# Kernel tuning notes

Hardware: AMD Instinct MI355X
Metric: run time of the kernel (lower is better)

Reference implementation:

```python
import jax, jax.numpy as jnp
import numpy as np

N_NODES = 100000
N_EDGES = 1250000
HID = 64
IN_CH = 64
OUT_CH = 16
N_GRAPHS = 512


def setup_inputs() -> dict:
    key = jax.random.key(0)
    ks = jax.random.split(key, 20)
    x = jax.random.normal(ks[0], (N_NODES, IN_CH), dtype=jnp.float32)
    edge_index = jax.random.randint(ks[1], (2, N_EDGES), 0, N_NODES, dtype=jnp.int64)
    batch = jnp.sort(jax.random.randint(ks[2], (N_NODES,), 0, N_GRAPHS, dtype=jnp.int64))
    s_in = 1.0 / np.sqrt(IN_CH)
    s_h = 1.0 / np.sqrt(HID)
    u = lambda k, shp, s: jax.random.uniform(k, shp, jnp.float32, -s, s)
    return {
        "x": x, "edge_index": edge_index, "batch": batch,
        "W0": u(ks[3], (IN_CH, HID), s_in), "b0": u(ks[4], (HID,), s_in),
        "W1a": u(ks[5], (HID, HID), s_h), "b1a": u(ks[6], (HID,), s_h),
        "W1b": u(ks[7], (HID, HID), s_h), "b1b": u(ks[8], (HID,), s_h),
        "W2a": u(ks[9], (HID, HID), s_h), "b2a": u(ks[10], (HID,), s_h),
        "W2b": u(ks[11], (HID, HID), s_h), "b2b": u(ks[12], (HID,), s_h),
        "W3a": u(ks[13], (HID, HID), s_h), "b3a": u(ks[14], (HID,), s_h),
        "W3b": u(ks[15], (HID, HID), s_h), "b3b": u(ks[16], (HID,), s_h),
        "Wl": u(ks[17], (HID, OUT_CH), s_h), "bl": u(ks[18], (OUT_CH,), s_h),
    }


def _gin_conv(h, src, dst, Wa, ba, Wb, bb):
    # GINConv, eps=0: mlp(x_i + sum_{j->i} x_j); mlp = Linear,ReLU,Linear
    agg = jax.ops.segment_sum(h[src], dst, num_segments=N_NODES)  # [N, HID]
    z = h + agg
    return jax.nn.relu(z @ Wa + ba) @ Wb + bb


def reference(x, edge_index, batch, W0, b0, W1a, b1a, W1b, b1b,
              W2a, b2a, W2b, b2b, W3a, b3a, W3b, b3b, Wl, bl):
    src, dst = edge_index[0], edge_index[1]
    h = jax.nn.relu(x @ W0 + b0)
    h = jax.nn.relu(_gin_conv(h, src, dst, W1a, b1a, W1b, b1b))
    h = jax.nn.relu(_gin_conv(h, src, dst, W2a, b2a, W2b, b2b))
    h = jax.nn.relu(_gin_conv(h, src, dst, W3a, b3a, W3b, b3b))
    # global mean pool over graphs
    sums = jax.ops.segment_sum(h, batch, num_segments=N_GRAPHS)  # [G, HID]
    cnts = jax.ops.segment_sum(jnp.ones((N_NODES,), h.dtype), batch, num_segments=N_GRAPHS)
    pooled = sums / jnp.maximum(cnts, 1.0)[:, None]
    # dropout p=0.5 is identity in eval mode
    return pooled @ Wl + bl  # [G, OUT_CH]
```

## Files before the change

### kernel.cpp

```cpp
#include <hip/hip_runtime.h>
#include <hip/hip_fp16.h>

#define N_NODES 100000
#define N_EDGES 1250000
#define HID 64
#define N_GRAPHS 512
#define OUT_CH 16

#define NSUP 196
#define SB_CAP 8192
#define E_BLK 2048
#define NPB ((N_EDGES + E_BLK - 1) / E_BLK)
#define TILE2 ((N_NODES + 127) / 128)
#define NWP 6
#define TSTRIDE 68
#define AGG_BLOCKS 3125

typedef _Float16 h16;
typedef _Float16 half2_t __attribute__((ext_vector_type(2)));
typedef _Float16 f16x8 __attribute__((ext_vector_type(8)));
typedef float f32x4 __attribute__((ext_vector_type(4)));

__device__ __forceinline__ void acc8(uint4 u, float* a) {
    half2_t h0 = __builtin_bit_cast(half2_t, u.x);
    half2_t h1 = __builtin_bit_cast(half2_t, u.y);
    half2_t h2 = __builtin_bit_cast(half2_t, u.z);
    half2_t h3 = __builtin_bit_cast(half2_t, u.w);
    a[0] += (float)h0[0]; a[1] += (float)h0[1];
    a[2] += (float)h1[0]; a[3] += (float)h1[1];
    a[4] += (float)h2[0]; a[5] += (float)h2[1];
    a[6] += (float)h3[0]; a[7] += (float)h3[1];
}

__device__ __forceinline__ unsigned pack2(float x, float y) {
    half2_t o;
    o[0] = (h16)x;
    o[1] = (h16)y;
    return __builtin_bit_cast(unsigned, o);
}

__global__ __launch_bounds__(256) void k_fat(const int* __restrict__ src,
                                             const int* __restrict__ dst,
                                             int* __restrict__ cnt,
                                             int* __restrict__ buckets,
                                             const float* __restrict__ W1a,
                                             const float* __restrict__ W1b,
                                             const float* __restrict__ W2a,
                                             const float* __restrict__ W2b,
                                             const float* __restrict__ W3a,
                                             const float* __restrict__ W3b,
                                             h16* __restrict__ WF,
                                             const float* __restrict__ W0,
                                             const float* __restrict__ B0,
                                             const float* __restrict__ Xin,
                                             h16* __restrict__ Hout) {
    __shared__ int hist[256];
    __shared__ int gbase[256];
    __shared__ int tsum[256];
    __shared__ __align__(16) int stage[E_BLK];
    __shared__ __align__(16) float sT[4 * 16 * TSTRIDE];

    int b = blockIdx.x;
    int t = threadIdx.x;

    if (b < NPB) {
        int e0 = b * E_BLK;
        int eN = N_EDGES - e0;
        if (eN > E_BLK) eN = E_BLK;

        hist[t] = 0;
        __syncthreads();
        for (int i = t; i < eN; i += 256) atomicAdd(&hist[dst[e0 + i] >> 9], 1);
        __syncthreads();

        int c = hist[t];
        tsum[t] = c;
        __syncthreads();
        for (int off = 1; off < 256; off <<= 1) {
            int u = (t >= off) ? tsum[t - off] : 0;
            __syncthreads();
            tsum[t] += u;
            __syncthreads();
        }
        int pref = tsum[t] - c;
        if (t < NSUP && c > 0) gbase[t] = atomicAdd(&cnt[t], c);
        hist[t] = pref;
        __syncthreads();

        for (int i = t; i < eN; i += 256) {
            int s = src[e0 + i];
            int d = dst[e0 + i];
            int p = atomicAdd(&hist[d >> 9], 1);
            stage[p] = ((d & 511) << 17) | s;
        }
        __syncthreads();

        if (t < NSUP && c > 0) {
            int lstart = hist[t] - c;
            int gb = gbase[t];
            int cap = SB_CAP - gb;
            int n = c < cap ? c : (cap > 0 ? cap : 0);
            int* dp = buckets + (size_t)t * SB_CAP + gb;
            int r = 0;
            while (r < n && (((size_t)(dp + r)) & 15)) { dp[r] = stage[lstart + r]; ++r; }
            for (; r + 4 <= n; r += 4) {
                int4 v;
                v.x = stage[lstart + r];
                v.y = stage[lstart + r + 1];
                v.z = stage[lstart + r + 2];
                v.w = stage[lstart + r + 3];
                *(int4*)(dp + r) = v;
            }
            for (; r < n; ++r) dp[r] = stage[lstart + r];
        }
    } else if (b < NPB + NWP) {
        const float* Ws[NWP] = {W1a, W1b, W2a, W2b, W3a, W3b};
        const float* W = Ws[b - NPB];
        h16* dstW = WF + (size_t)(b - NPB) * 4096;
#pragma unroll
        for (int i = 0; i < 16; ++i) {
            int s = t + 256 * i;
            int k = s >> 6, col = s & 63;
            int kc = k >> 5, quad = (k >> 3) & 3, j = k & 7;
            int c = col >> 4, n = col & 15;
            dstW[((c * 2 + kc) * 4 + quad) * 128 + n * 8 + j] = (h16)W[s];
        }
    } else {
        int lb = b - NPB - NWP;
        int w = t >> 6, lane = t & 63;
        int n16 = lane & 15, quad = lane >> 4;
        float* T = sT + w * 16 * TSTRIDE;

        f16x8 bw[4][2];
#pragma unroll
        for (int c = 0; c < 4; ++c)
#pragma unroll
            for (int kc = 0; kc < 2; ++kc) {
                f16x8 v;
#pragma unroll
                for (int j = 0; j < 8; ++j)
                    v[j] = (h16)W0[(kc * 32 + quad * 8 + j) * 64 + c * 16 + n16];
                bw[c][kc] = v;
            }
        float bv[4];
#pragma unroll
        for (int c = 0; c < 4; ++c) bv[c] = B0[c * 16 + n16];

#pragma unroll
        for (int tt = 0; tt < 2; ++tt) {
            int rbase = lb * 128 + tt * 64 + w * 16;
            int arow = rbase + n16;
            int crow = arow < N_NODES ? arow : N_NODES - 1;
            f16x8 a[2];
#pragma unroll
            for (int kc = 0; kc < 2; ++kc) {
                const float4* xp = (const float4*)(Xin + (size_t)crow * HID + kc * 32 + quad * 8);
                float4 p = xp[0], q = xp[1];
                f16x8 v;
                v[0] = (h16)p.x; v[1] = (h16)p.y; v[2] = (h16)p.z; v[3] = (h16)p.w;
                v[4] = (h16)q.x; v[5] = (h16)q.y; v[6] = (h16)q.z; v[7] = (h16)q.w;
                a[kc] = v;
            }

            f32x4 acc[4];
#pragma unroll
            for (int c = 0; c < 4; ++c) {
                acc[c] = (f32x4){bv[c], bv[c], bv[c], bv[c]};
#pragma unroll
                for (int kc = 0; kc < 2; ++kc)
                    acc[c] = __builtin_amdgcn_mfma_f32_16x16x32_f16(a[kc], bw[c][kc], acc[c], 0, 0, 0);
            }

#pragma unroll
            for (int c = 0; c < 4; ++c)
#pragma unroll
                for (int r = 0; r < 4; ++r)
                    T[(quad * 4 + r) * TSTRIDE + c * 16 + n16] = fmaxf(acc[c][r], 0.f);
            {
                int rl = lane >> 2, seg = lane & 3;
                int row = rbase + rl;
                if (row < N_NODES) {
                    const float* tr = &T[rl * TSTRIDE + seg * 16];
                    f16x8 o0, o1;
#pragma unroll
                    for (int i = 0; i < 8; ++i) {
                        o0[i] = (h16)tr[i];
                        o1[i] = (h16)tr[8 + i];
                    }
                    f16x8* dp = (f16x8*)(Hout + (size_t)row * HID + seg * 16);
                    dp[0] = o0;
                    dp[1] = o1;
                }
            }
        }
    }
}

__global__ __launch_bounds__(256) void k_sort(const int* __restrict__ cnt,
                                              int* __restrict__ buckets,
                                              int* __restrict__ rowptrS) {
    __shared__ int srt[SB_CAP];
    __shared__ int hist[512];
    __shared__ int curs[512];
    __shared__ int tsum[256];
    int s = blockIdx.x, t = threadIdx.x;
    int n = cnt[s];
    n = n < SB_CAP ? n : SB_CAP;
    int* gb = buckets + (size_t)s * SB_CAP;
    int sBase = s * SB_CAP;

    hist[t] = 0;
    hist[t + 256] = 0;
    __syncthreads();
    for (int i = t; i < n; i += 256) atomicAdd(&hist[gb[i] >> 17], 1);
    __syncthreads();

    int c0 = hist[2 * t], c1 = hist[2 * t + 1];
    int tot = c0 + c1;
    tsum[t] = tot;
    __syncthreads();
    for (int off = 1; off < 256; off <<= 1) {
        int u = (t >= off) ? tsum[t - off] : 0;
        __syncthreads();
        tsum[t] += u;
        __syncthreads();
    }
    int pref = tsum[t] - tot;
    curs[2 * t] = pref;
    curs[2 * t + 1] = pref + c0;
    rowptrS[s * 513 + 2 * t] = sBase + pref;
    rowptrS[s * 513 + 2 * t + 1] = sBase + pref + c0;
    if (t == 255) rowptrS[s * 513 + 512] = sBase + n;
    __syncthreads();

    for (int i = t; i < n; i += 256) {
        int rec = gb[i];
        int pos = atomicAdd(&curs[rec >> 17], 1);
        srt[pos] = rec;
    }
    __syncthreads();
    for (int i = t; i < n; i += 256) gb[i] = srt[i];
}

__global__ __launch_bounds__(256) void k_aggregate(const int* __restrict__ rowptrS,
                                                   const int* __restrict__ buckets,
                                                   const h16* __restrict__ H,
                                                   h16* __restrict__ Z) {
    const uint4* H8 = (const uint4*)H;
    uint4* Z8 = (uint4*)Z;
    int lane = threadIdx.x & 63;
    int part = lane >> 3, sub = lane & 7;
    int gwave = (blockIdx.x * 256 + threadIdx.x) >> 6;
    int nw = (gridDim.x * 256) >> 6;
    for (int i0 = gwave * 8; i0 < N_NODES; i0 += nw * 8) {
        int i = i0 + part;
        bool valid = i < N_NODES;
        int iv = valid ? i : N_NODES - 1;
        int s = iv >> 9, l = iv & 511;
        int start = rowptrS[s * 513 + l];
        int end = valid ? rowptrS[s * 513 + l + 1] : start;
        float a[8] = {0.f, 0.f, 0.f, 0.f, 0.f, 0.f, 0.f, 0.f};
        acc8(H8[(size_t)iv * 8 + sub], a);
        int j = start;
        for (; j + 8 <= end; j += 8) {
            int s0 = buckets[j] & 0x1FFFF;
            int s1 = buckets[j + 1] & 0x1FFFF;
            int s2 = buckets[j + 2] & 0x1FFFF;
            int s3 = buckets[j + 3] & 0x1FFFF;
            int s4 = buckets[j + 4] & 0x1FFFF;
            int s5 = buckets[j + 5] & 0x1FFFF;
            int s6 = buckets[j + 6] & 0x1FFFF;
            int s7 = buckets[j + 7] & 0x1FFFF;
            uint4 u0 = H8[(size_t)s0 * 8 + sub];
            uint4 u1 = H8[(size_t)s1 * 8 + sub];
            uint4 u2 = H8[(size_t)s2 * 8 + sub];
            uint4 u3 = H8[(size_t)s3 * 8 + sub];
            uint4 u4 = H8[(size_t)s4 * 8 + sub];
            uint4 u5 = H8[(size_t)s5 * 8 + sub];
            uint4 u6 = H8[(size_t)s6 * 8 + sub];
            uint4 u7 = H8[(size_t)s7 * 8 + sub];
            acc8(u0, a);
            acc8(u1, a);
            acc8(u2, a);
            acc8(u3, a);
            acc8(u4, a);
            acc8(u5, a);
            acc8(u6, a);
            acc8(u7, a);
        }
        if (j + 4 <= end) {
            int s0 = buckets[j] & 0x1FFFF;
            int s1 = buckets[j + 1] & 0x1FFFF;
            int s2 = buckets[j + 2] & 0x1FFFF;
            int s3 = buckets[j + 3] & 0x1FFFF;
            uint4 u0 = H8[(size_t)s0 * 8 + sub];
            uint4 u1 = H8[(size_t)s1 * 8 + sub];
            uint4 u2 = H8[(size_t)s2 * 8 + sub];
            uint4 u3 = H8[(size_t)s3 * 8 + sub];
            acc8(u0, a);
            acc8(u1, a);
            acc8(u2, a);
            acc8(u3, a);
            j += 4;
        }
        if (j + 2 <= end) {
            int s0 = buckets[j] & 0x1FFFF;
            int s1 = buckets[j + 1] & 0x1FFFF;
            uint4 u0 = H8[(size_t)s0 * 8 + sub];
            uint4 u1 = H8[(size_t)s1 * 8 + sub];
            acc8(u0, a);
            acc8(u1, a);
            j += 2;
        }
        if (j < end) {
            int s0 = buckets[j] & 0x1FFFF;
            acc8(H8[(size_t)s0 * 8 + sub], a);
        }
        if (valid) {
            uint4 o;
            o.x = pack2(a[0], a[1]);
            o.y = pack2(a[2], a[3]);
            o.z = pack2(a[4], a[5]);
            o.w = pack2(a[6], a[7]);
            Z8[(size_t)i * 8 + sub] = o;
        }
    }
}

__global__ __launch_bounds__(256) void k_mlp(const h16* __restrict__ WaF,
                                             const float* __restrict__ Ba,
                                             const h16* __restrict__ WbF,
                                             const float* __restrict__ Bb,
                                             const h16* __restrict__ Zin,
                                             h16* __restrict__ Hout) {
    __shared__ __align__(16) float sT[4 * 16 * TSTRIDE];
    int t = threadIdx.x;
    int w = t >> 6, lane = t & 63;
    int n16 = lane & 15, quad = lane >> 4;
    float* T = sT + w * 16 * TSTRIDE;

    f16x8 bwa[4][2], bwb[4][2];
#pragma unroll
    for (int c = 0; c < 4; ++c)
#pragma unroll
        for (int kc = 0; kc < 2; ++kc) {
            int f = ((c * 2 + kc) * 4 + quad) * 128 + n16 * 8;
            bwa[c][kc] = *(const f16x8*)(WaF + f);
            bwb[c][kc] = *(const f16x8*)(WbF + f);
        }
    float bva[4], bvb[4];
#pragma unroll
    for (int c = 0; c < 4; ++c) {
        bva[c] = Ba[c * 16 + n16];
        bvb[c] = Bb[c * 16 + n16];
    }

#pragma unroll
    for (int tt = 0; tt < 2; ++tt) {
        int rbase = blockIdx.x * 128 + tt * 64 + w * 16;
        int arow = rbase + n16;
        int crow = arow < N_NODES ? arow : N_NODES - 1;
        const f16x8* zp = (const f16x8*)(Zin + (size_t)crow * HID + quad * 8);
        f16x8 a0 = zp[0];
        f16x8 a1 = zp[4];

        f32x4 acc[4];
#pragma unroll
        for (int c = 0; c < 4; ++c) {
            acc[c] = (f32x4){bva[c], bva[c], bva[c], bva[c]};
            acc[c] = __builtin_amdgcn_mfma_f32_16x16x32_f16(a0, bwa[c][0], acc[c], 0, 0, 0);
            acc[c] = __builtin_amdgcn_mfma_f32_16x16x32_f16(a1, bwa[c][1], acc[c], 0, 0, 0);
        }

#pragma unroll
        for (int c = 0; c < 4; ++c)
#pragma unroll
            for (int r = 0; r < 4; ++r)
                T[(quad * 4 + r) * TSTRIDE + c * 16 + n16] = fmaxf(acc[c][r], 0.f);

        f16x8 ta[2];
#pragma unroll
        for (int kc = 0; kc < 2; ++kc) {
            float4 p = *(const float4*)&T[n16 * TSTRIDE + kc * 32 + quad * 8];
            float4 q = *(const float4*)&T[n16 * TSTRIDE + kc * 32 + quad * 8 + 4];
            f16x8 v;
            v[0] = (h16)p.x; v[1] = (h16)p.y; v[2] = (h16)p.z; v[3] = (h16)p.w;
            v[4] = (h16)q.x; v[5] = (h16)q.y; v[6] = (h16)q.z; v[7] = (h16)q.w;
            ta[kc] = v;
        }

#pragma unroll
        for (int c = 0; c < 4; ++c) {
            acc[c] = (f32x4){bvb[c], bvb[c], bvb[c], bvb[c]};
            acc[c] = __builtin_amdgcn_mfma_f32_16x16x32_f16(ta[0], bwb[c][0], acc[c], 0, 0, 0);
            acc[c] = __builtin_amdgcn_mfma_f32_16x16x32_f16(ta[1], bwb[c][1], acc[c], 0, 0, 0);
        }

#pragma unroll
        for (int c = 0; c < 4; ++c)
#pragma unroll
            for (int r = 0; r < 4; ++r)
                T[(quad * 4 + r) * TSTRIDE + c * 16 + n16] = fmaxf(acc[c][r], 0.f);
        {
            int rl = lane >> 2, seg = lane & 3;
            int row = rbase + rl;
            if (row < N_NODES) {
                const float* tr = &T[rl * TSTRIDE + seg * 16];
                f16x8 o0, o1;
#pragma unroll
                for (int i = 0; i < 8; ++i) {
                    o0[i] = (h16)tr[i];
                    o1[i] = (h16)tr[8 + i];
                }
                f16x8* dp = (f16x8*)(Hout + (size_t)row * HID + seg * 16);
                dp[0] = o0;
                dp[1] = o1;
            }
        }
    }
}

__global__ __launch_bounds__(256) void k_poolfinal(const h16* __restrict__ H,
                                                   const int* __restrict__ batch,
                                                   const float* __restrict__ Wl,
                                                   const float* __restrict__ bl,
                                                   float* __restrict__ out) {
    __shared__ float sp[4 * HID];
    int g = blockIdx.x;
    int t = threadIdx.x;
    int lane = t & 63, w = t >> 6;
    int lo = 0, hi = N_NODES;
    while (lo < hi) { int m = (lo + hi) >> 1; if (batch[m] < g) lo = m + 1; else hi = m; }
    int start = lo;
    hi = N_NODES;
    while (lo < hi) { int m = (lo + hi) >> 1; if (batch[m] < g + 1) lo = m + 1; else hi = m; }
    int end = lo;
    float s0 = 0.f, s1 = 0.f, s2 = 0.f, s3 = 0.f;
    int r = start + w;
    for (; r + 12 < end; r += 16) {
        float v0 = (float)H[(size_t)r * HID + lane];
        float v1 = (float)H[(size_t)(r + 4) * HID + lane];
        float v2 = (float)H[(size_t)(r + 8) * HID + lane];
        float v3 = (float)H[(size_t)(r + 12) * HID + lane];
        s0 += v0; s1 += v1; s2 += v2; s3 += v3;
    }
    for (; r < end; r += 4) s0 += (float)H[(size_t)r * HID + lane];
    sp[w * HID + lane] = s0 + s1 + s2 + s3;
    __syncthreads();
    if (t < HID) {
        float tot = sp[t] + sp[HID + t] + sp[2 * HID + t] + sp[3 * HID + t];
        float c = (end > start) ? (float)(end - start) : 1.0f;
        sp[t] = tot / c;
    }
    __syncthreads();
    if (t < OUT_CH) {
        float acc = bl[t];
#pragma unroll
        for (int k = 0; k < HID; ++k) acc += sp[k] * Wl[k * OUT_CH + t];
        out[g * OUT_CH + t] = acc;
    }
}

extern "C" void kernel_launch(void* const* d_in, const int* in_sizes, int n_in,
                              void* d_out, int out_size, void* d_ws, size_t ws_size,
                              hipStream_t stream) {
    const float* x     = (const float*)d_in[0];
    const int*   edge  = (const int*)d_in[1];
    const int*   batch = (const int*)d_in[2];
    const float* W0  = (const float*)d_in[3];
    const float* b0  = (const float*)d_in[4];
    const float* W1a = (const float*)d_in[5];
    const float* b1a = (const float*)d_in[6];
    const float* W1b = (const float*)d_in[7];
    const float* b1b = (const float*)d_in[8];
    const float* W2a = (const float*)d_in[9];
    const float* b2a = (const float*)d_in[10];
    const float* W2b = (const float*)d_in[11];
    const float* b2b = (const float*)d_in[12];
    const float* W3a = (const float*)d_in[13];
    const float* b3a = (const float*)d_in[14];
    const float* W3b = (const float*)d_in[15];
    const float* b3b = (const float*)d_in[16];
    const float* Wl  = (const float*)d_in[17];
    const float* bl  = (const float*)d_in[18];
    float* out = (float*)d_out;

    const int* src = edge;
    const int* dst = edge + N_EDGES;

    h16* HA = (h16*)d_ws;
    h16* Z  = HA + (size_t)N_NODES * HID;
    int* cnt     = (int*)(Z + (size_t)N_NODES * HID);
    int* rowptrS = cnt + NSUP;
    int* buckets = rowptrS + NSUP * 513;
    h16* WF      = (h16*)(buckets + (size_t)NSUP * SB_CAP);
    h16* W1aF = WF;
    h16* W1bF = WF + 4096 * 1;
    h16* W2aF = WF + 4096 * 2;
    h16* W2bF = WF + 4096 * 3;
    h16* W3aF = WF + 4096 * 4;
    h16* W3bF = WF + 4096 * 5;

    hipMemsetAsync(cnt, 0, NSUP * sizeof(int), stream);
    k_fat<<<NPB + NWP + TILE2, 256, 0, stream>>>(src, dst, cnt, buckets,
        W1a, W1b, W2a, W2b, W3a, W3b, WF, W0, b0, x, HA);
    k_sort<<<NSUP, 256, 0, stream>>>(cnt, buckets, rowptrS);

    k_aggregate<<<AGG_BLOCKS, 256, 0, stream>>>(rowptrS, buckets, HA, Z);
    k_mlp<<<TILE2, 256, 0, stream>>>(W1aF, b1a, W1bF, b1b, Z, HA);

    k_aggregate<<<AGG_BLOCKS, 256, 0, stream>>>(rowptrS, buckets, HA, Z);
    k_mlp<<<TILE2, 256, 0, stream>>>(W2aF, b2a, W2bF, b2b, Z, HA);

    k_aggregate<<<AGG_BLOCKS, 256, 0, stream>>>(rowptrS, buckets, HA, Z);
    k_mlp<<<TILE2, 256, 0, stream>>>(W3aF, b3a, W3bF, b3b, Z, HA);

    k_poolfinal<<<N_GRAPHS, 256, 0, stream>>>(HA, batch, Wl, bl, out);
}
```

Measured before the change: 274.6 us.

## Split first-layer features into column quarters for cache-local gather aggregation

The first hidden activation is now written as four 16-feature column slabs instead of row-major rows. A new quarter-wise aggregation kernel gathers each slab separately, so each pass's random gather touches a much smaller working set and can stay cache-resident. The first MLP reads this split layout through a new flag. Later layers keep the row-major path. The cost is more waves each doing smaller 32-byte gathers, plus repeated index reads across the four quarters.

Result: slower. 298.3 us (+8.6%).

```diff
diff --git a/kernel.cpp b/kernel.cpp
--- a/kernel.cpp
+++ b/kernel.cpp
@@ -15,6 +15,7 @@
 #define NWP 6
 #define TSTRIDE 68
 #define AGG_BLOCKS 3125
+#define QCHUNKS 3125
 
 typedef _Float16 h16;
 typedef _Float16 half2_t __attribute__((ext_vector_type(2)));
@@ -187,9 +188,9 @@
                         o0[i] = (h16)tr[i];
                         o1[i] = (h16)tr[8 + i];
                     }
-                    f16x8* dp = (f16x8*)(Hout + (size_t)row * HID + seg * 16);
-                    dp[0] = o0;
-                    dp[1] = o1;
+                    h16* dp = Hout + (size_t)seg * N_NODES * 16 + (size_t)row * 16;
+                    *(f16x8*)dp = o0;
+                    *(f16x8*)(dp + 8) = o1;
                 }
             }
         }
@@ -240,6 +241,77 @@
     }
     __syncthreads();
     for (int i = t; i < n; i += 256) gb[i] = srt[i];
+}
+
+__global__ __launch_bounds__(256) void k_aggregate_q(const int* __restrict__ rowptrS,
+                                                     const int* __restrict__ buckets,
+                                                     const h16* __restrict__ Hq,
+                                                     h16* __restrict__ Zq) {
+    const uint4* H2 = (const uint4*)Hq;
+    uint4* Z2 = (uint4*)Zq;
+    int lane = threadIdx.x & 63;
+    int sub = lane & 1;
+    int grp = lane >> 1;
+    int gwave = (blockIdx.x * 256 + threadIdx.x) >> 6;
+    int q = gwave / QCHUNKS;
+    int i = (gwave - q * QCHUNKS) * 32 + grp;
+    size_t pb = (size_t)q * N_NODES * 2;
+    int s = i >> 9, l = i & 511;
+    int start = rowptrS[s * 513 + l];
+    int end = rowptrS[s * 513 + l + 1];
+    float a[8] = {0.f, 0.f, 0.f, 0.f, 0.f, 0.f, 0.f, 0.f};
+    acc8(H2[pb + (size_t)i * 2 + sub], a);
+    int j = start;
+    for (; j + 8 <= end; j += 8) {
+        int s0 = buckets[j] & 0x1FFFF;
+        int s1 = buckets[j + 1] & 0x1FFFF;
+        int s2 = buckets[j + 2] & 0x1FFFF;
+        int s3 = buckets[j + 3] & 0x1FFFF;
+        int s4 = buckets[j + 4] & 0x1FFFF;
+        int s5 = buckets[j + 5] & 0x1FFFF;
+        int s6 = buckets[j + 6] & 0x1FFFF;
+        int s7 = buckets[j + 7] & 0x1FFFF;
+        uint4 u0 = H2[pb + (size_t)s0 * 2 + sub];
+        uint4 u1 = H2[pb + (size_t)s1 * 2 + sub];
+        uint4 u2 = H2[pb + (size_t)s2 * 2 + sub];
+        uint4 u3 = H2[pb + (size_t)s3 * 2 + sub];
+        uint4 u4 = H2[pb + (size_t)s4 * 2 + sub];
+        uint4 u5 = H2[pb + (size_t)s5 * 2 + sub];
+        uint4 u6 = H2[pb + (size_t)s6 * 2 + sub];
+        uint4 u7 = H2[pb + (size_t)s7 * 2 + sub];
+        acc8(u0, a); acc8(u1, a); acc8(u2, a); acc8(u3, a);
+        acc8(u4, a); acc8(u5, a); acc8(u6, a); acc8(u7, a);
+    }
+    if (j + 4 <= end) {
+        int s0 = buckets[j] & 0x1FFFF;
+        int s1 = buckets[j + 1] & 0x1FFFF;
+        int s2 = buckets[j + 2] & 0x1FFFF;
+        int s3 = buckets[j + 3] & 0x1FFFF;
+        uint4 u0 = H2[pb + (size_t)s0 * 2 + sub];
+        uint4 u1 = H2[pb + (size_t)s1 * 2 + sub];
+        uint4 u2 = H2[pb + (size_t)s2 * 2 + sub];
+        uint4 u3 = H2[pb + (size_t)s3 * 2 + sub];
+        acc8(u0, a); acc8(u1, a); acc8(u2, a); acc8(u3, a);
+        j += 4;
+    }
+    if (j + 2 <= end) {
+        int s0 = buckets[j] & 0x1FFFF;
+        int s1 = buckets[j + 1] & 0x1FFFF;
+        uint4 u0 = H2[pb + (size_t)s0 * 2 + sub];
+        uint4 u1 = H2[pb + (size_t)s1 * 2 + sub];
+        acc8(u0, a); acc8(u1, a);
+        j += 2;
+    }
+    if (j < end) {
+        int s0 = buckets[j] & 0x1FFFF;
+        acc8(H2[pb + (size_t)s0 * 2 + sub], a);
+    }
+    uint4 o;
+    o.x = pack2(a[0], a[1]);
+    o.y = pack2(a[2], a[3]);
+    o.z = pack2(a[4], a[5]);
+    o.w = pack2(a[6], a[7]);
+    Z2[pb + (size_t)i * 2 + sub] = o;
 }
 
 __global__ __launch_bounds__(256) void k_aggregate(const int* __restrict__ rowptrS,
@@ -332,7 +404,8 @@
                                              const h16* __restrict__ WbF,
                                              const float* __restrict__ Bb,
                                              const h16* __restrict__ Zin,
-                                             h16* __restrict__ Hout) {
+                                             h16* __restrict__ Hout,
+                                             const int qin) {
     __shared__ __align__(16) float sT[4 * 16 * TSTRIDE];
     int t = threadIdx.x;
     int w = t >> 6, lane = t & 63;
@@ -360,9 +433,16 @@
         int rbase = blockIdx.x * 128 + tt * 64 + w * 16;
         int arow = rbase + n16;
         int crow = arow < N_NODES ? arow : N_NODES - 1;
-        const f16x8* zp = (const f16x8*)(Zin + (size_t)crow * HID + quad * 8);
-        f16x8 a0 = zp[0];
-        f16x8 a1 = zp[4];
+        f16x8 a0, a1;
+        if (qin) {
+            size_t off = (size_t)(quad >> 1) * N_NODES * 16 + (size_t)crow * 16 + (quad & 1) * 8;
+            a0 = *(const f16x8*)(Zin + off);
+            a1 = *(const f16x8*)(Zin + (size_t)2 * N_NODES * 16 + off);
+        } else {
+            const f16x8* zp = (const f16x8*)(Zin + (size_t)crow * HID + quad * 8);
+            a0 = zp[0];
+            a1 = zp[4];
+        }
 
         f32x4 acc[4];
 #pragma unroll
@@ -506,14 +586,14 @@
         W1a, W1b, W2a, W2b, W3a, W3b, WF, W0, b0, x, HA);
     k_sort<<<NSUP, 256, 0, stream>>>(cnt, buckets, rowptrS);
 
+    k_aggregate_q<<<AGG_BLOCKS, 256, 0, stream>>>(rowptrS, buckets, HA, Z);
+    k_mlp<<<TILE2, 256, 0, stream>>>(W1aF, b1a, W1bF, b1b, Z, HA, 1);
+
     k_aggregate<<<AGG_BLOCKS, 256, 0, stream>>>(rowptrS, buckets, HA, Z);
-    k_mlp<<<TILE2, 256, 0, stream>>>(W1aF, b1a, W1bF, b1b, Z, HA);
+    k_mlp<<<TILE2, 256, 0, stream>>>(W2aF, b2a, W2bF, b2b, Z, HA, 0);
 
     k_aggregate<<<AGG_BLOCKS, 256, 0, stream>>>(rowptrS, buckets, HA, Z);
-    k_mlp<<<TILE2, 256, 0, stream>>>(W2aF, b2a, W2bF, b2b, Z, HA);
-
-    k_aggregate<<<AGG_BLOCKS, 256, 0, stream>>>(rowptrS, buckets, HA, Z);
-    k_mlp<<<TILE2, 256, 0, stream>>>(W3aF, b3a, W3bF, b3b, Z, HA);
+    k_mlp<<<TILE2, 256, 0, stream>>>(W3aF, b3a, W3bF, b3b, Z, HA, 0);
 
     k_poolfinal<<<N_GRAPHS, 256, 0, stream>>>(HA, batch, Wl, bl, out);
 }
```
